# Kernel tuning notes

Hardware: AMD Instinct MI355X
Metric: run time of the kernel (lower is better)

The kernel has to match this reference:

```python
import jax, jax.numpy as jnp
import numpy as np

N_TAGS = 32
START_IDX = 30  # tag_vocabulary['<START>']
STOP_IDX = 31   # tag_vocabulary['<STOP>']
NEG = -10000.0  # CRF_CONSTRAINT_VALUE
T = 65536


def setup_inputs() -> dict:
    key = jax.random.key(0)
    k1, k2 = jax.random.split(key)
    chunk_features = jax.random.normal(k1, (T, N_TAGS), dtype=jnp.float32)
    # learned transition matrix with START/STOP constraints applied as in __init__
    transitions = jax.random.normal(k2, (N_TAGS, N_TAGS), dtype=jnp.float32)
    transitions = transitions.at[START_IDX, :].set(NEG).at[:, STOP_IDX].set(NEG)
    # initial forward-variable state: -1e4 everywhere except START tag
    init_alphas = jnp.full((N_TAGS,), NEG, dtype=jnp.float32).at[START_IDX].set(0.0)
    return {"chunk_features": chunk_features, "transitions": transitions, "init_alphas": init_alphas}


def reference(chunk_features, transitions, init_alphas):
    # CRF forward algorithm (log partition function) via scan over time.
    # step: next[i, j] = alphas[j] + transitions[i, j] + emit[i]; alphas' = LSE_j next
    def step(alphas, emit):
        next_tag_vars = alphas[None, :] + transitions + emit[:, None]  # [K, K]
        return jax.nn.logsumexp(next_tag_vars, axis=-1), None

    alphas, _ = jax.lax.scan(step, init_alphas, chunk_features)
    terminal = alphas + transitions[STOP_IDX]  # [K]
    return jax.nn.logsumexp(terminal)[None]  # shape (1,), matching torch output
```

## Files before the change

kernel.cpp:

```cpp
#include <hip/hip_runtime.h>
#include <hip/hip_bf16.h>

#define NT 32
#define START_TAG 30
#define STOP_TAG 31
#define L2E 1.4426950408889634f
#define LN2 0.6931471805599453f
#define FW 8

typedef unsigned short u16;
typedef __attribute__((ext_vector_type(8))) short short8;
typedef __attribute__((ext_vector_type(16))) float f32x16;

__device__ __forceinline__ int fexp_of(float m) {
  return (int)((__float_as_uint(m) >> 23) & 255u) - 126;
}

__device__ __forceinline__ unsigned pk_bf16(float lo, float hi) {
  unsigned r;
  asm("v_cvt_pk_bf16_f32 %0, %1, %2" : "=v"(r) : "v"(lo), "v"(hi));
  return r;
}

__device__ __forceinline__ int SIG(int k) {
  return (k & 3) + 8 * ((k >> 2) & 1) + 4 * ((k >> 3) & 1) + 16 * (k >> 4);
}
__device__ __forceinline__ int RHO(int r, int h) {
  return (r & 3) + 8 * (r >> 2) + 4 * h;
}

__device__ __forceinline__ f32x16 mfma2(short8 a0, short8 a1, short8 b0, short8 b1) {
  f32x16 z = {};
  f32x16 d = __builtin_amdgcn_mfma_f32_32x32x16_bf16(a0, b0, z, 0, 0, 0);
  return __builtin_amdgcn_mfma_f32_32x32x16_bf16(a1, b1, d, 0, 0, 0);
}

__device__ __forceinline__ void store_mat(u16* __restrict__ wm, float* __restrict__ wo,
                                          float* __restrict__ wx, const float m[16],
                                          float offs, int h, int c, int lane) {
  __hip_bfloat16* bm = (__hip_bfloat16*)wm;
#pragma unroll
  for (int r = 0; r < 16; ++r)
    bm[RHO(r, h) * NT + SIG(c)] = __float2bfloat16(m[r]);
  if (h == 0) wo[c] = offs;
  float mx = offs;
#pragma unroll
  for (int d = 32; d; d >>= 1) mx = fmaxf(mx, __shfl_xor(mx, d, 64));
  if (lane == 0) wx[0] = mx;
}

struct Chain {
  short8 b0, b1;
  float m[16];
  float offs;
};

__device__ __forceinline__ void k1_step(Chain& ch, const float* __restrict__ e,
                                        short8 pa0, short8 pa1, int h, bool rn) {
  const float4* e4 = (const float4*)e;
  float4 e0 = e4[h], e1 = e4[2 + h], e2 = e4[4 + h], e3 = e4[6 + h];
  f32x16 d = mfma2(pa0, pa1, ch.b0, ch.b1);
  ch.m[0] = d[0] * e0.x;  ch.m[1] = d[1] * e0.y;  ch.m[2] = d[2] * e0.z;  ch.m[3] = d[3] * e0.w;
  ch.m[4] = d[4] * e1.x;  ch.m[5] = d[5] * e1.y;  ch.m[6] = d[6] * e1.z;  ch.m[7] = d[7] * e1.w;
  ch.m[8] = d[8] * e2.x;  ch.m[9] = d[9] * e2.y;  ch.m[10] = d[10] * e2.z; ch.m[11] = d[11] * e2.w;
  ch.m[12] = d[12] * e3.x; ch.m[13] = d[13] * e3.y; ch.m[14] = d[14] * e3.z; ch.m[15] = d[15] * e3.w;
  if (rn) {
    float cm = ch.m[0];
#pragma unroll
    for (int i = 1; i < 16; ++i) cm = fmaxf(cm, ch.m[i]);
    cm = fmaxf(cm, __shfl_xor(cm, 32, 64));
    int ex = fexp_of(cm);
    ch.offs += (float)ex;
#pragma unroll
    for (int i = 0; i < 16; ++i) ch.m[i] = ldexpf(ch.m[i], -ex);
  }
  union { unsigned u[4]; short8 s; } B0, B1;
#pragma unroll
  for (int p = 0; p < 4; ++p) {
    B0.u[p] = pk_bf16(ch.m[2 * p], ch.m[2 * p + 1]);
    B1.u[p] = pk_bf16(ch.m[8 + 2 * p], ch.m[8 + 2 * p + 1]);
  }
  ch.b0 = B0.s; ch.b1 = B1.s;
}

__device__ __forceinline__ void init_identity(Chain& ch, int h, int c) {
  union { unsigned u[4]; short8 s; } B0, B1;
#pragma unroll
  for (int p = 0; p < 4; ++p) {
    unsigned lo0 = (SIG(8 * h + 2 * p) == c) ? 0x3F80u : 0u;
    unsigned hi0 = (SIG(8 * h + 2 * p + 1) == c) ? 0x3F80u : 0u;
    B0.u[p] = lo0 | (hi0 << 16);
    unsigned lo1 = (SIG(16 + 8 * h + 2 * p) == c) ? 0x3F80u : 0u;
    unsigned hi1 = (SIG(16 + 8 * h + 2 * p + 1) == c) ? 0x3F80u : 0u;
    B1.u[p] = lo1 | (hi1 << 16);
  }
  ch.b0 = B0.s; ch.b1 = B1.s; ch.offs = 0.f;
#pragma unroll
  for (int i = 0; i < 16; ++i) ch.m[i] = 0.f;
}

template <int LCH>
__global__ __launch_bounds__(256) void crf_k1(
    const float* __restrict__ feat, const float* __restrict__ trans,
    u16* __restrict__ wm, float* __restrict__ wo, float* __restrict__ wx) {
  __shared__ __align__(16) float E[8 * LCH * NT];
  const int tid = threadIdx.x, lane = tid & 63, w = tid >> 6;
  const int h = lane >> 5, c = lane & 31;

  const float4* src = (const float4*)(feat + (size_t)blockIdx.x * 8 * LCH * NT);
  float4* dst = (float4*)E;
#pragma unroll
  for (int kk = 0; kk < LCH / 4; ++kk) {
    int k = tid + kk * 256;
    float4 v = src[k];
    v.x = exp2f(v.x * L2E); v.y = exp2f(v.y * L2E);
    v.z = exp2f(v.z * L2E); v.w = exp2f(v.w * L2E);
    dst[k] = v;
  }

  short8 pa0, pa1;
  {
    union { unsigned u[4]; short8 s; } A0, A1;
#pragma unroll
    for (int p = 0; p < 4; ++p) {
      float g00 = exp2f(trans[c * NT + SIG(8 * h + 2 * p)] * L2E);
      float g01 = exp2f(trans[c * NT + SIG(8 * h + 2 * p + 1)] * L2E);
      float g10 = exp2f(trans[c * NT + SIG(16 + 8 * h + 2 * p)] * L2E);
      float g11 = exp2f(trans[c * NT + SIG(16 + 8 * h + 2 * p + 1)] * L2E);
      A0.u[p] = pk_bf16(g00, g01);
      A1.u[p] = pk_bf16(g10, g11);
    }
    pa0 = A0.s; pa1 = A1.s;
  }
  __syncthreads();

  Chain ch0, ch1;
  init_identity(ch0, h, c);
  init_identity(ch1, h, c);
  const float* eb0 = E + (size_t)(2 * w) * LCH * NT;
  const float* eb1 = E + (size_t)(2 * w + 1) * LCH * NT;
#pragma unroll
  for (int s = 0; s < LCH; s += 4) {
#pragma unroll
    for (int t = 0; t < 4; ++t) {
      const bool rn = (t == 3);
      k1_step(ch0, eb0 + (s + t) * NT, pa0, pa1, h, rn);
      k1_step(ch1, eb1 + (s + t) * NT, pa0, pa1, h, rn);
    }
  }

  const int c0 = blockIdx.x * 8 + 2 * w;
  store_mat(wm + (size_t)c0 * 1024, wo + (size_t)c0 * NT, wx + c0,
            ch0.m, ch0.offs, h, c, lane);
  store_mat(wm + (size_t)(c0 + 1) * 1024, wo + (size_t)(c0 + 1) * NT, wx + c0 + 1,
            ch1.m, ch1.offs, h, c, lane);
}

__device__ __forceinline__ void gprod(
    const u16* __restrict__ sm, const float* __restrict__ so,
    const float* __restrict__ sx, int c0, int grp, int h, int c,
    float m[16], float& offs) {
#pragma unroll
  for (int r = 0; r < 16; ++r) m[r] = (RHO(r, h) == c) ? 1.f : 0.f;
  offs = 0.f;

#pragma unroll 4
  for (int gg = 0; gg < grp; ++gg) {
    const u16* rowp = sm + (size_t)(c0 + gg) * 1024 + c * NT;
    short8 a0 = *(const short8*)(rowp + 8 * h);
    short8 a1 = *(const short8*)(rowp + 16 + 8 * h);
    const float* O = so + (size_t)(c0 + gg) * NT;
    const float mmax = sx[c0 + gg];
    const float4* o4 = (const float4*)O;
    float4 w0 = o4[h], w1 = o4[2 + h], w2 = o4[4 + h], w3 = o4[6 + h];
    float t[16];
    t[0]  = ldexpf(m[0],  (int)(w0.x - mmax)); t[1]  = ldexpf(m[1],  (int)(w0.y - mmax));
    t[2]  = ldexpf(m[2],  (int)(w0.z - mmax)); t[3]  = ldexpf(m[3],  (int)(w0.w - mmax));
    t[4]  = ldexpf(m[4],  (int)(w1.x - mmax)); t[5]  = ldexpf(m[5],  (int)(w1.y - mmax));
    t[6]  = ldexpf(m[6],  (int)(w1.z - mmax)); t[7]  = ldexpf(m[7],  (int)(w1.w - mmax));
    t[8]  = ldexpf(m[8],  (int)(w2.x - mmax)); t[9]  = ldexpf(m[9],  (int)(w2.y - mmax));
    t[10] = ldexpf(m[10], (int)(w2.z - mmax)); t[11] = ldexpf(m[11], (int)(w2.w - mmax));
    t[12] = ldexpf(m[12], (int)(w3.x - mmax)); t[13] = ldexpf(m[13], (int)(w3.y - mmax));
    t[14] = ldexpf(m[14], (int)(w3.z - mmax)); t[15] = ldexpf(m[15], (int)(w3.w - mmax));

    union { unsigned u[4]; short8 s; } B0, B1;
#pragma unroll
    for (int p = 0; p < 4; ++p) {
      B0.u[p] = pk_bf16(t[2 * p], t[2 * p + 1]);
      B1.u[p] = pk_bf16(t[8 + 2 * p], t[8 + 2 * p + 1]);
    }
    f32x16 d = mfma2(a0, a1, B0.s, B1.s);
    float cm = d[0];
#pragma unroll
    for (int i = 1; i < 16; ++i) cm = fmaxf(cm, d[i]);
    cm = fmaxf(cm, __shfl_xor(cm, 32, 64));
    int ex = fexp_of(cm);
#pragma unroll
    for (int i = 0; i < 16; ++i) m[i] = ldexpf(d[i], -ex);
    offs += mmax + (float)ex;
  }
}

__global__ __launch_bounds__(64) void crf_kc(
    const u16* __restrict__ sm, const float* __restrict__ so,
    const float* __restrict__ sx, u16* __restrict__ dm,
    float* __restrict__ dof, float* __restrict__ dx, int grp) {
  const int lane = threadIdx.x;
  const int h = lane >> 5, c = lane & 31;
  const int g = blockIdx.x;
  float m[16], offs;
  gprod(sm, so, sx, g * grp, grp, h, c, m, offs);
  store_mat(dm + (size_t)g * 1024, dof + (size_t)g * NT, dx + g, m, offs, h, c, lane);
}

__global__ __launch_bounds__(512) void crf_k3g(
    const u16* __restrict__ sm, const float* __restrict__ so,
    const float* __restrict__ sx, const float* __restrict__ trans,
    float* __restrict__ out, int n1) {
  const int tid = threadIdx.x, w = tid >> 6, lane = tid & 63;
  const int h = lane >> 5, c = lane & 31;
  __shared__ __align__(16) float Gls[FW][NT * NT];
  __shared__ __align__(16) float Ools[FW][NT];
  __shared__ float Xls[FW];

  {
    const int per = n1 / FW;
    float m[16], offs;
    gprod(sm, so, sx, w * per, per, h, c, m, offs);
#pragma unroll
    for (int r = 0; r < 16; ++r) Gls[w][RHO(r, h) * NT + c] = m[r];
    if (h == 0) Ools[w][c] = offs;
    float mx = offs;
#pragma unroll
    for (int d = 32; d; d >>= 1) mx = fmaxf(mx, __shfl_xor(mx, d, 64));
    if (lane == 0) Xls[w] = mx;
  }
  __syncthreads();

  if (w == 0) {
    float g[16], go;
#pragma unroll
    for (int r = 0; r < 16; ++r) g[r] = Gls[0][RHO(r, h) * NT + c];
    go = Ools[0][c];

    for (int gg = 1; gg < FW; ++gg) {
      float af[16];
#pragma unroll
      for (int i = 0; i < 8; ++i) {
        af[i]     = Gls[gg][c * NT + SIG(8 * h + i)];
        af[8 + i] = Gls[gg][c * NT + SIG(16 + 8 * h + i)];
      }
      const float mmax = Xls[gg];
      float t[16];
#pragma unroll
      for (int r = 0; r < 16; ++r)
        t[r] = ldexpf(g[r], (int)(Ools[gg][RHO(r, h)] - mmax));

      union { unsigned u[4]; short8 s; } A0, A1, B0, B1;
#pragma unroll
      for (int p = 0; p < 4; ++p) {
        A0.u[p] = pk_bf16(af[2 * p], af[2 * p + 1]);
        A1.u[p] = pk_bf16(af[8 + 2 * p], af[8 + 2 * p + 1]);
        B0.u[p] = pk_bf16(t[2 * p], t[2 * p + 1]);
        B1.u[p] = pk_bf16(t[8 + 2 * p], t[8 + 2 * p + 1]);
      }
      f32x16 d = mfma2(A0.s, A1.s, B0.s, B1.s);
      float cm = d[0];
#pragma unroll
      for (int i = 1; i < 16; ++i) cm = fmaxf(cm, d[i]);
      cm = fmaxf(cm, __shfl_xor(cm, 32, 64));
      int ex = fexp_of(cm);
#pragma unroll
      for (int i = 0; i < 16; ++i) g[i] = ldexpf(d[i], -ex);
      go += mmax + (float)ex;
    }

    float ts[16];
    float tm = -1e30f;
#pragma unroll
    for (int r = 0; r < 16; ++r) {
      ts[r] = trans[STOP_TAG * NT + RHO(r, h)] * L2E;
      tm = fmaxf(tm, ts[r]);
    }
    tm = fmaxf(tm, __shfl_xor(tm, 32, 64));
    float s = 0.f;
#pragma unroll
    for (int r = 0; r < 16; ++r) s += g[r] * exp2f(ts[r] - tm);
    s += __shfl_xor(s, 32, 64);
    if (lane == START_TAG) out[0] = (go + tm + log2f(s)) * LN2;
  }
}

extern "C" void kernel_launch(void* const* d_in, const int* in_sizes, int n_in,
                              void* d_out, int out_size, void* d_ws, size_t ws_size,
                              hipStream_t stream) {
  const float* feat = (const float*)d_in[0];
  const float* trans = (const float*)d_in[1];
  float* out = (float*)d_out;

  const int T = in_sizes[0] / NT;

  int C = 2048;
  for (;;) {
    const size_t n1t = (size_t)C / 16;
    const size_t need = (size_t)C * 2048 + (size_t)C * 128 + (size_t)C * 4 +
                        n1t * 2048 + n1t * 128 + n1t * 4 + 4096;
    if (C <= 512) break;
    if (need <= ws_size && (T % C) == 0 && ((T / C) % 4) == 0 &&
        (C % 256) == 0 && (n1t % FW) == 0 && (T / C) <= 64)
      break;
    C >>= 1;
  }
  const int lch = T / C;
  const int n1 = C / 16;

  char* p = (char*)d_ws;
  u16* wm = (u16*)p;     p += (size_t)C * 2048;
  float* wo = (float*)p; p += (size_t)C * 128;
  float* wx = (float*)p; p += (size_t)C * 4;
  u16* l1m = (u16*)p;    p += (size_t)n1 * 2048;
  float* l1o = (float*)p; p += (size_t)n1 * 128;
  float* l1x = (float*)p;

  if (lch == 16)
    crf_k1<16><<<C / 8, 256, 0, stream>>>(feat, trans, wm, wo, wx);
  else if (lch == 32)
    crf_k1<32><<<C / 8, 256, 0, stream>>>(feat, trans, wm, wo, wx);
  else
    crf_k1<64><<<C / 8, 256, 0, stream>>>(feat, trans, wm, wo, wx);

  crf_kc<<<n1, 64, 0, stream>>>(wm, wo, wx, l1m, l1o, l1x, 16);
  crf_k3g<<<1, 512, 0, stream>>>(l1m, l1o, l1x, trans, out, n1);
}
```

Before: 42.54 us.

## Fuse CRF chunk scan and reduction tree into one cooperative kernel

For T=65536, a single cooperative launch of 256 blocks replaces the multi-kernel pipeline. Each block scans its 8 chunks of 32 steps, combines the 8 chunk matrices in shared memory, and only then writes one matrix per block. Two grid syncs then run the 16-way and final reductions. This removes several kernel launches and most global workspace traffic, at the cost of grid-wide barriers and idle blocks during the later reduction stages.

```diff
diff --git a/kernel.cpp b/kernel.cpp
--- a/kernel.cpp
+++ b/kernel.cpp
@@ -1,5 +1,8 @@
 #include <hip/hip_runtime.h>
+#include <hip/hip_cooperative_groups.h>
 #include <hip/hip_bf16.h>
+
+namespace cg = cooperative_groups;
 
 #define NT 32
 #define START_TAG 30
@@ -97,63 +100,6 @@
   ch.b0 = B0.s; ch.b1 = B1.s; ch.offs = 0.f;
 #pragma unroll
   for (int i = 0; i < 16; ++i) ch.m[i] = 0.f;
-}
-
-template <int LCH>
-__global__ __launch_bounds__(256) void crf_k1(
-    const float* __restrict__ feat, const float* __restrict__ trans,
-    u16* __restrict__ wm, float* __restrict__ wo, float* __restrict__ wx) {
-  __shared__ __align__(16) float E[8 * LCH * NT];
-  const int tid = threadIdx.x, lane = tid & 63, w = tid >> 6;
-  const int h = lane >> 5, c = lane & 31;
-
-  const float4* src = (const float4*)(feat + (size_t)blockIdx.x * 8 * LCH * NT);
-  float4* dst = (float4*)E;
-#pragma unroll
-  for (int kk = 0; kk < LCH / 4; ++kk) {
-    int k = tid + kk * 256;
-    float4 v = src[k];
-    v.x = exp2f(v.x * L2E); v.y = exp2f(v.y * L2E);
-    v.z = exp2f(v.z * L2E); v.w = exp2f(v.w * L2E);
-    dst[k] = v;
-  }
-
-  short8 pa0, pa1;
-  {
-    union { unsigned u[4]; short8 s; } A0, A1;
-#pragma unroll
-    for (int p = 0; p < 4; ++p) {
-      float g00 = exp2f(trans[c * NT + SIG(8 * h + 2 * p)] * L2E);
-      float g01 = exp2f(trans[c * NT + SIG(8 * h + 2 * p + 1)] * L2E);
-      float g10 = exp2f(trans[c * NT + SIG(16 + 8 * h + 2 * p)] * L2E);
-      float g11 = exp2f(trans[c * NT + SIG(16 + 8 * h + 2 * p + 1)] * L2E);
-      A0.u[p] = pk_bf16(g00, g01);
-      A1.u[p] = pk_bf16(g10, g11);
-    }
-    pa0 = A0.s; pa1 = A1.s;
-  }
-  __syncthreads();
-
-  Chain ch0, ch1;
-  init_identity(ch0, h, c);
-  init_identity(ch1, h, c);
-  const float* eb0 = E + (size_t)(2 * w) * LCH * NT;
-  const float* eb1 = E + (size_t)(2 * w + 1) * LCH * NT;
-#pragma unroll
-  for (int s = 0; s < LCH; s += 4) {
-#pragma unroll
-    for (int t = 0; t < 4; ++t) {
-      const bool rn = (t == 3);
-      k1_step(ch0, eb0 + (s + t) * NT, pa0, pa1, h, rn);
-      k1_step(ch1, eb1 + (s + t) * NT, pa0, pa1, h, rn);
-    }
-  }
-
-  const int c0 = blockIdx.x * 8 + 2 * w;
-  store_mat(wm + (size_t)c0 * 1024, wo + (size_t)c0 * NT, wx + c0,
-            ch0.m, ch0.offs, h, c, lane);
-  store_mat(wm + (size_t)(c0 + 1) * 1024, wo + (size_t)(c0 + 1) * NT, wx + c0 + 1,
-            ch1.m, ch1.offs, h, c, lane);
 }
 
 __device__ __forceinline__ void gprod(
@@ -201,6 +147,215 @@
   }
 }
 
+__global__ __launch_bounds__(256) void crf_coop(
+    const float* __restrict__ feat, const float* __restrict__ trans,
+    float* __restrict__ out,
+    u16* __restrict__ bm, float* __restrict__ bo, float* __restrict__ bx,
+    u16* __restrict__ l1m, float* __restrict__ l1o, float* __restrict__ l1x) {
+  const int LCH = 32;
+  cg::grid_group grid = cg::this_grid();
+  const int tid = threadIdx.x, lane = tid & 63, w = tid >> 6;
+  const int h = lane >> 5, c = lane & 31;
+  const int bid = blockIdx.x;
+
+  __shared__ __align__(16) float shbuf[8 * 1024];
+  __shared__ __align__(16) float Ools[8][NT];
+  __shared__ float Xls[8];
+
+  {
+    const float4* src = (const float4*)(feat + (size_t)bid * 8 * LCH * NT);
+    float4* dst = (float4*)shbuf;
+#pragma unroll
+    for (int kk = 0; kk < LCH / 4; ++kk) {
+      int k = tid + kk * 256;
+      float4 v = src[k];
+      v.x = exp2f(v.x * L2E); v.y = exp2f(v.y * L2E);
+      v.z = exp2f(v.z * L2E); v.w = exp2f(v.w * L2E);
+      dst[k] = v;
+    }
+  }
+
+  short8 pa0, pa1;
+  {
+    union { unsigned u[4]; short8 s; } A0, A1;
+#pragma unroll
+    for (int p = 0; p < 4; ++p) {
+      float g00 = exp2f(trans[c * NT + SIG(8 * h + 2 * p)] * L2E);
+      float g01 = exp2f(trans[c * NT + SIG(8 * h + 2 * p + 1)] * L2E);
+      float g10 = exp2f(trans[c * NT + SIG(16 + 8 * h + 2 * p)] * L2E);
+      float g11 = exp2f(trans[c * NT + SIG(16 + 8 * h + 2 * p + 1)] * L2E);
+      A0.u[p] = pk_bf16(g00, g01);
+      A1.u[p] = pk_bf16(g10, g11);
+    }
+    pa0 = A0.s; pa1 = A1.s;
+  }
+  __syncthreads();
+
+  {
+    Chain ch0, ch1;
+    init_identity(ch0, h, c);
+    init_identity(ch1, h, c);
+    const float* eb0 = shbuf + (size_t)(2 * w) * LCH * NT;
+    const float* eb1 = shbuf + (size_t)(2 * w + 1) * LCH * NT;
+#pragma unroll
+    for (int s = 0; s < LCH; s += 4) {
+#pragma unroll
+      for (int t = 0; t < 4; ++t) {
+        const bool rn = (t == 3);
+        k1_step(ch0, eb0 + (s + t) * NT, pa0, pa1, h, rn);
+        k1_step(ch1, eb1 + (s + t) * NT, pa0, pa1, h, rn);
+      }
+    }
+    float* G0 = shbuf + (size_t)(2 * w) * 1024;
+    float* G1 = shbuf + (size_t)(2 * w + 1) * 1024;
+#pragma unroll
+    for (int r = 0; r < 16; ++r) {
+      G0[RHO(r, h) * NT + c] = ch0.m[r];
+      G1[RHO(r, h) * NT + c] = ch1.m[r];
+    }
+    if (h == 0) { Ools[2 * w][c] = ch0.offs; Ools[2 * w + 1][c] = ch1.offs; }
+    float mx0 = ch0.offs, mx1 = ch1.offs;
+#pragma unroll
+    for (int d = 32; d; d >>= 1) {
+      mx0 = fmaxf(mx0, __shfl_xor(mx0, d, 64));
+      mx1 = fmaxf(mx1, __shfl_xor(mx1, d, 64));
+    }
+    if (lane == 0) { Xls[2 * w] = mx0; Xls[2 * w + 1] = mx1; }
+  }
+  __syncthreads();
+
+  if (w == 0) {
+    float g[16], go;
+#pragma unroll
+    for (int r = 0; r < 16; ++r) g[r] = shbuf[RHO(r, h) * NT + c];
+    go = Ools[0][c];
+
+    for (int gg = 1; gg < 8; ++gg) {
+      const float* Gg = shbuf + (size_t)gg * 1024;
+      float af[16];
+#pragma unroll
+      for (int i = 0; i < 8; ++i) {
+        af[i]     = Gg[c * NT + SIG(8 * h + i)];
+        af[8 + i] = Gg[c * NT + SIG(16 + 8 * h + i)];
+      }
+      const float mmax = Xls[gg];
+      float t[16];
+#pragma unroll
+      for (int r = 0; r < 16; ++r)
+        t[r] = ldexpf(g[r], (int)(Ools[gg][RHO(r, h)] - mmax));
+
+      union { unsigned u[4]; short8 s; } A0, A1, B0, B1;
+#pragma unroll
+      for (int p = 0; p < 4; ++p) {
+        A0.u[p] = pk_bf16(af[2 * p], af[2 * p + 1]);
+        A1.u[p] = pk_bf16(af[8 + 2 * p], af[8 + 2 * p + 1]);
+        B0.u[p] = pk_bf16(t[2 * p], t[2 * p + 1]);
+        B1.u[p] = pk_bf16(t[8 + 2 * p], t[8 + 2 * p + 1]);
+      }
+      f32x16 d = mfma2(A0.s, A1.s, B0.s, B1.s);
+      float cm = d[0];
+#pragma unroll
+      for (int i = 1; i < 16; ++i) cm = fmaxf(cm, d[i]);
+      cm = fmaxf(cm, __shfl_xor(cm, 32, 64));
+      int ex = fexp_of(cm);
+#pragma unroll
+      for (int i = 0; i < 16; ++i) g[i] = ldexpf(d[i], -ex);
+      go += mmax + (float)ex;
+    }
+    store_mat(bm + (size_t)bid * 1024, bo + (size_t)bid * NT, bx + bid,
+              g, go, h, c, lane);
+  }
+
+  __threadfence();
+  grid.sync();
+
+  if (bid < 16 && w == 0) {
+    float m[16], offs;
+    gprod(bm, bo, bx, bid * 16, 16, h, c, m, offs);
+    store_mat(l1m + (size_t)bid * 1024, l1o + (size_t)bid * NT, l1x + bid,
+              m, offs, h, c, lane);
+  }
+
+  __threadfence();
+  grid.sync();
+
+  if (bid == 0 && w == 0) {
+    float m[16], offs;
+    gprod(l1m, l1o, l1x, 0, 16, h, c, m, offs);
+
+    float ts[16];
+    float tm = -1e30f;
+#pragma unroll
+    for (int r = 0; r < 16; ++r) {
+      ts[r] = trans[STOP_TAG * NT + RHO(r, h)] * L2E;
+      tm = fmaxf(tm, ts[r]);
+    }
+    tm = fmaxf(tm, __shfl_xor(tm, 32, 64));
+    float s = 0.f;
+#pragma unroll
+    for (int r = 0; r < 16; ++r) s += m[r] * exp2f(ts[r] - tm);
+    s += __shfl_xor(s, 32, 64);
+    if (lane == START_TAG) out[0] = (offs + tm + log2f(s)) * LN2;
+  }
+}
+
+template <int LCH>
+__global__ __launch_bounds__(256) void crf_k1(
+    const float* __restrict__ feat, const float* __restrict__ trans,
+    u16* __restrict__ wm, float* __restrict__ wo, float* __restrict__ wx) {
+  __shared__ __align__(16) float E[8 * LCH * NT];
+  const int tid = threadIdx.x, lane = tid & 63, w = tid >> 6;
+  const int h = lane >> 5, c = lane & 31;
+
+  const float4* src = (const float4*)(feat + (size_t)blockIdx.x * 8 * LCH * NT);
+  float4* dst = (float4*)E;
+#pragma unroll
+  for (int kk = 0; kk < LCH / 4; ++kk) {
+    int k = tid + kk * 256;
+    float4 v = src[k];
+    v.x = exp2f(v.x * L2E); v.y = exp2f(v.y * L2E);
+    v.z = exp2f(v.z * L2E); v.w = exp2f(v.w * L2E);
+    dst[k] = v;
+  }
+
+  short8 pa0, pa1;
+  {
+    union { unsigned u[4]; short8 s; } A0, A1;
+#pragma unroll
+    for (int p = 0; p < 4; ++p) {
+      float g00 = exp2f(trans[c * NT + SIG(8 * h + 2 * p)] * L2E);
+      float g01 = exp2f(trans[c * NT + SIG(8 * h + 2 * p + 1)] * L2E);
+      float g10 = exp2f(trans[c * NT + SIG(16 + 8 * h + 2 * p)] * L2E);
+      float g11 = exp2f(trans[c * NT + SIG(16 + 8 * h + 2 * p + 1)] * L2E);
+      A0.u[p] = pk_bf16(g00, g01);
+      A1.u[p] = pk_bf16(g10, g11);
+    }
+    pa0 = A0.s; pa1 = A1.s;
+  }
+  __syncthreads();
+
+  Chain ch0, ch1;
+  init_identity(ch0, h, c);
+  init_identity(ch1, h, c);
+  const float* eb0 = E + (size_t)(2 * w) * LCH * NT;
+  const float* eb1 = E + (size_t)(2 * w + 1) * LCH * NT;
+#pragma unroll
+  for (int s = 0; s < LCH; s += 4) {
+#pragma unroll
+    for (int t = 0; t < 4; ++t) {
+      const bool rn = (t == 3);
+      k1_step(ch0, eb0 + (s + t) * NT, pa0, pa1, h, rn);
+      k1_step(ch1, eb1 + (s + t) * NT, pa0, pa1, h, rn);
+    }
+  }
+
+  const int c0 = blockIdx.x * 8 + 2 * w;
+  store_mat(wm + (size_t)c0 * 1024, wo + (size_t)c0 * NT, wx + c0,
+            ch0.m, ch0.offs, h, c, lane);
+  store_mat(wm + (size_t)(c0 + 1) * 1024, wo + (size_t)(c0 + 1) * NT, wx + c0 + 1,
+            ch1.m, ch1.offs, h, c, lane);
+}
+
 __global__ __launch_bounds__(64) void crf_kc(
     const u16* __restrict__ sm, const float* __restrict__ so,
     const float* __restrict__ sx, u16* __restrict__ dm,
@@ -300,6 +455,23 @@
 
   const int T = in_sizes[0] / NT;
 
+  if (T == 65536) {
+    char* p = (char*)d_ws;
+    u16* bm = (u16*)p;     p += (size_t)256 * 2048;
+    float* bo = (float*)p; p += (size_t)256 * 128;
+    float* bx = (float*)p; p += (size_t)256 * 4;
+    u16* l1m = (u16*)p;    p += (size_t)16 * 2048;
+    float* l1o = (float*)p; p += (size_t)16 * 128;
+    float* l1x = (float*)p;
+
+    void* args[] = {(void*)&feat, (void*)&trans, (void*)&out,
+                    (void*)&bm, (void*)&bo, (void*)&bx,
+                    (void*)&l1m, (void*)&l1o, (void*)&l1x};
+    hipLaunchCooperativeKernel((const void*)crf_coop, dim3(256), dim3(256),
+                               args, 0, stream);
+    return;
+  }
+
   int C = 2048;
   for (;;) {
     const size_t n1t = (size_t)C / 16;
```

After: 132.7 us. 3.12x slower.
